# Optimization experiments

Hardware: AMD Instinct MI355X
Metric: run time of the kernel (lower is better)

## Reference

```python
import jax, jax.numpy as jnp
import numpy as np

B, C, H, W = 8, 64, 256, 256
SQ = 256  # max(int(64*16*0.25),1)

def setup_inputs() -> dict:
    key = jax.random.key(0)
    k1, k2, k3, k4, k5 = jax.random.split(key, 5)
    t = jax.random.normal(k1, (B, C, H, W), dtype=jnp.float32)
    reduce_w = jax.random.normal(k2, (SQ, 16 * C), dtype=jnp.float32) * (1.0 / np.sqrt(16 * C))
    reduce_b = jax.random.normal(k3, (SQ,), dtype=jnp.float32) * 0.01
    expand_w = jax.random.normal(k4, (16 * C, SQ), dtype=jnp.float32) * (1.0 / np.sqrt(SQ))
    expand_b = jax.random.normal(k5, (16 * C,), dtype=jnp.float32) * 0.01
    return {"t": t, "reduce_w": reduce_w, "reduce_b": reduce_b,
            "expand_w": expand_w, "expand_b": expand_b}

def _mish(x):
    return x * jnp.tanh(jax.nn.softplus(x))

def reference(t, reduce_w, reduce_b, expand_w, expand_b):
    b, c, h, w = t.shape  # h, w assumed multiples of 4 (no pad needed)
    gh, gw = h // 4, w // 4
    # split into 4x4 grid of patches: [B, C, 4, gh, 4, gw]
    tg = t.reshape(b, c, 4, gh, 4, gw)
    # global avg pool per patch -> [B, C, 4, 4]; reorder to cat order (i*4+j)*C + c
    pooled = tg.mean(axis=(3, 5))                      # [B, C, 4, 4]
    pooled = pooled.transpose(0, 2, 3, 1).reshape(b, 16 * c)  # [B, 16C]
    # squeeze-excite MLP (1x1 convs on [B,16C,1,1] == linear layers)
    s = _mish(pooled @ reduce_w.T + reduce_b)          # [B, SQ]
    g = jax.nn.sigmoid(s @ expand_w.T + expand_b)      # [B, 16C]
    # gates back to grid: [B, 4, 4, C] -> [B, C, 4, 1, 4, 1]
    gates = g.reshape(b, 4, 4, c).transpose(0, 3, 1, 2)[:, :, :, None, :, None]
    out = (tg * gates).reshape(b, c, h, w)
    return out
```

## Files before the change

kernel.cpp:

```cpp
#include <hip/hip_runtime.h>
#include <math.h>


#define Bsz 8
#define Csz 64
#define Hsz 256
#define Wsz 256
#define SQsz 256
#define C16 1024

__global__ __launch_bounds__(256) void pool_kernel(const float* __restrict__ t,
                                                   float* __restrict__ pooled) {
    int bid = blockIdx.x;
    int p   = bid & 15;
    int bc  = bid >> 4;
    int i   = p >> 2, j = p & 3;
    const float* base = t + (((size_t)bc * Hsz + (size_t)i * 64) * Wsz + (size_t)j * 64);
    int tid = threadIdx.x;
    float sum = 0.f;
#pragma unroll
    for (int k = 0; k < 4; ++k) {
        int g    = tid + k * 256;
        int row  = g >> 4;
        int col4 = g & 15;
        float4 v = *(const float4*)(base + (size_t)row * Wsz + col4 * 4);
        sum += v.x + v.y + v.z + v.w;
    }
#pragma unroll
    for (int off = 32; off > 0; off >>= 1) sum += __shfl_down(sum, off, 64);
    __shared__ float wsum[4];
    if ((tid & 63) == 0) wsum[tid >> 6] = sum;
    __syncthreads();
    if (tid == 0) {
        float s = wsum[0] + wsum[1] + wsum[2] + wsum[3];
        int b = bc >> 6;
        int c = bc & 63;
        pooled[b * C16 + p * Csz + c] = s * (1.0f / 4096.0f);
    }
}

__global__ __launch_bounds__(64) void reduce_kernel(const float* __restrict__ pooled,
                                                    const float* __restrict__ reduce_w,
                                                    const float* __restrict__ reduce_b,
                                                    float* __restrict__ s_out) {
    int o = blockIdx.x;
    int l = threadIdx.x;
    const float* wrow = reduce_w + (size_t)o * C16;
    float acc[Bsz] = {0.f, 0.f, 0.f, 0.f, 0.f, 0.f, 0.f, 0.f};
#pragma unroll
    for (int m = 0; m < 16; ++m) {
        int k = l + 64 * m;
        float wv = wrow[k];
#pragma unroll
        for (int b = 0; b < Bsz; ++b)
            acc[b] = fmaf(wv, pooled[b * C16 + k], acc[b]);
    }
#pragma unroll
    for (int off = 32; off > 0; off >>= 1) {
#pragma unroll
        for (int b = 0; b < Bsz; ++b)
            acc[b] += __shfl_xor(acc[b], off, 64);
    }
    if (l < Bsz) {
        float x = acc[l] + reduce_b[o];
        float sp = (x > 15.f) ? x : log1pf(expf(x));
        s_out[l * SQsz + o] = x * tanhf(sp);
    }
}

__global__ __launch_bounds__(64) void expand_kernel(const float* __restrict__ s_in,
                                                    const float* __restrict__ expand_w,
                                                    const float* __restrict__ expand_b,
                                                    float* __restrict__ g_out) {
    int o = blockIdx.x;
    int l = threadIdx.x;
    const float* wrow = expand_w + (size_t)o * SQsz;
    float acc[Bsz] = {0.f, 0.f, 0.f, 0.f, 0.f, 0.f, 0.f, 0.f};
#pragma unroll
    for (int m = 0; m < 4; ++m) {
        int k = l + 64 * m;
        float wv = wrow[k];
#pragma unroll
        for (int b = 0; b < Bsz; ++b)
            acc[b] = fmaf(wv, s_in[b * SQsz + k], acc[b]);
    }
#pragma unroll
    for (int off = 32; off > 0; off >>= 1) {
#pragma unroll
        for (int b = 0; b < Bsz; ++b)
            acc[b] += __shfl_xor(acc[b], off, 64);
    }
    if (l < Bsz) {
        float x = acc[l] + expand_b[o];
        g_out[l * C16 + o] = 1.0f / (1.0f + expf(-x));
    }
}

__global__ __launch_bounds__(256) void scale_kernel(const float* __restrict__ t,
                                                    const float* __restrict__ g,
                                                    float* __restrict__ out) {
    unsigned int idx = blockIdx.x * 256u + threadIdx.x;
    int w4 = idx & 63;
    int h  = (idx >> 6) & 255;
    int c  = (idx >> 14) & 63;
    int b  = idx >> 20;
    int p  = ((h >> 6) << 2) | (w4 >> 4);
    float gate = g[(b << 10) + (p << 6) + c];
    float4 v = *(const float4*)(t + (size_t)idx * 4);
    float4 r;
    r.x = v.x * gate;
    r.y = v.y * gate;
    r.z = v.z * gate;
    r.w = v.w * gate;
    *(float4*)(out + (size_t)idx * 4) = r;
}

extern "C" void kernel_launch(void* const* d_in, const int* in_sizes, int n_in,
                              void* d_out, int out_size, void* d_ws, size_t ws_size,
                              hipStream_t stream) {
    const float* t        = (const float*)d_in[0];
    const float* reduce_w = (const float*)d_in[1];
    const float* reduce_b = (const float*)d_in[2];
    const float* expand_w = (const float*)d_in[3];
    const float* expand_b = (const float*)d_in[4];
    float* out = (float*)d_out;

    float* pooled = (float*)d_ws;
    float* s_buf  = pooled + Bsz * C16;
    float* g_buf  = s_buf + Bsz * SQsz;

    pool_kernel  <<<Bsz * Csz * 16, 256, 0, stream>>>(t, pooled);
    reduce_kernel<<<SQsz,            64, 0, stream>>>(pooled, reduce_w, reduce_b, s_buf);
    expand_kernel<<<C16,             64, 0, stream>>>(s_buf, expand_w, expand_b, g_buf);
    scale_kernel <<<32768,          256, 0, stream>>>(t, g_buf, out);
}
```

Measured before the change: 257.5 us.

## Widen MLP kernels to one thread per input and use nontemporal scale loads/stores

The reduce and expand matvec kernels now give each thread a single input element (1024 and 256 threads per block) and combine the per-wave partial sums through shared memory, instead of running a serial 16- or 4-step loop in one wave. This shortens per-block latency on these small serial stages. The scale kernel switches to nontemporal vector loads and stores for the streamed tensor, so it is meant to pollute the cache less. The trade-off is that the input tensor may already be cached from the pooling pass, and nontemporal loads could bypass that reuse.

After: 260.4 us. Within noise of the previous version (+1.1%).

```diff
diff --git a/kernel.cpp b/kernel.cpp
--- a/kernel.cpp
+++ b/kernel.cpp
@@ -8,6 +8,8 @@
 #define Wsz 256
 #define SQsz 256
 #define C16 1024
+
+typedef float f32x4 __attribute__((ext_vector_type(4)));
 
 __global__ __launch_bounds__(256) void pool_kernel(const float* __restrict__ t,
                                                    float* __restrict__ pooled) {
@@ -23,7 +25,7 @@
         int g    = tid + k * 256;
         int row  = g >> 4;
         int col4 = g & 15;
-        float4 v = *(const float4*)(base + (size_t)row * Wsz + col4 * 4);
+        f32x4 v = *(const f32x4*)(base + (size_t)row * Wsz + col4 * 4);
         sum += v.x + v.y + v.z + v.w;
     }
 #pragma unroll
@@ -39,60 +41,68 @@
     }
 }
 
-__global__ __launch_bounds__(64) void reduce_kernel(const float* __restrict__ pooled,
-                                                    const float* __restrict__ reduce_w,
-                                                    const float* __restrict__ reduce_b,
-                                                    float* __restrict__ s_out) {
-    int o = blockIdx.x;
-    int l = threadIdx.x;
-    const float* wrow = reduce_w + (size_t)o * C16;
-    float acc[Bsz] = {0.f, 0.f, 0.f, 0.f, 0.f, 0.f, 0.f, 0.f};
+__global__ __launch_bounds__(1024) void reduce_kernel(const float* __restrict__ pooled,
+                                                      const float* __restrict__ reduce_w,
+                                                      const float* __restrict__ reduce_b,
+                                                      float* __restrict__ s_out) {
+    int o   = blockIdx.x;
+    int tid = threadIdx.x;
+    int w   = tid >> 6;
+    int l   = tid & 63;
+    float wv = reduce_w[(size_t)o * C16 + tid];
+    float acc[Bsz];
 #pragma unroll
-    for (int m = 0; m < 16; ++m) {
-        int k = l + 64 * m;
-        float wv = wrow[k];
-#pragma unroll
-        for (int b = 0; b < Bsz; ++b)
-            acc[b] = fmaf(wv, pooled[b * C16 + k], acc[b]);
-    }
+    for (int b = 0; b < Bsz; ++b)
+        acc[b] = wv * pooled[b * C16 + tid];
 #pragma unroll
     for (int off = 32; off > 0; off >>= 1) {
 #pragma unroll
         for (int b = 0; b < Bsz; ++b)
             acc[b] += __shfl_xor(acc[b], off, 64);
     }
-    if (l < Bsz) {
-        float x = acc[l] + reduce_b[o];
+    __shared__ float red[16][Bsz];
+    if (l == 0) {
+#pragma unroll
+        for (int b = 0; b < Bsz; ++b) red[w][b] = acc[b];
+    }
+    __syncthreads();
+    if (tid < Bsz) {
+        float x = reduce_b[o];
+#pragma unroll
+        for (int q = 0; q < 16; ++q) x += red[q][tid];
         float sp = (x > 15.f) ? x : log1pf(expf(x));
-        s_out[l * SQsz + o] = x * tanhf(sp);
+        s_out[tid * SQsz + o] = x * tanhf(sp);
     }
 }
 
-__global__ __launch_bounds__(64) void expand_kernel(const float* __restrict__ s_in,
-                                                    const float* __restrict__ expand_w,
-                                                    const float* __restrict__ expand_b,
-                                                    float* __restrict__ g_out) {
-    int o = blockIdx.x;
-    int l = threadIdx.x;
-    const float* wrow = expand_w + (size_t)o * SQsz;
-    float acc[Bsz] = {0.f, 0.f, 0.f, 0.f, 0.f, 0.f, 0.f, 0.f};
+__global__ __launch_bounds__(256) void expand_kernel(const float* __restrict__ s_in,
+                                                     const float* __restrict__ expand_w,
+                                                     const float* __restrict__ expand_b,
+                                                     float* __restrict__ g_out) {
+    int o   = blockIdx.x;
+    int tid = threadIdx.x;
+    int w   = tid >> 6;
+    int l   = tid & 63;
+    float wv = expand_w[(size_t)o * SQsz + tid];
+    float acc[Bsz];
 #pragma unroll
-    for (int m = 0; m < 4; ++m) {
-        int k = l + 64 * m;
-        float wv = wrow[k];
-#pragma unroll
-        for (int b = 0; b < Bsz; ++b)
-            acc[b] = fmaf(wv, s_in[b * SQsz + k], acc[b]);
-    }
+    for (int b = 0; b < Bsz; ++b)
+        acc[b] = wv * s_in[b * SQsz + tid];
 #pragma unroll
     for (int off = 32; off > 0; off >>= 1) {
 #pragma unroll
         for (int b = 0; b < Bsz; ++b)
             acc[b] += __shfl_xor(acc[b], off, 64);
     }
-    if (l < Bsz) {
-        float x = acc[l] + expand_b[o];
-        g_out[l * C16 + o] = 1.0f / (1.0f + expf(-x));
+    __shared__ float red[4][Bsz];
+    if (l == 0) {
+#pragma unroll
+        for (int b = 0; b < Bsz; ++b) red[w][b] = acc[b];
+    }
+    __syncthreads();
+    if (tid < Bsz) {
+        float x = expand_b[o] + red[0][tid] + red[1][tid] + red[2][tid] + red[3][tid];
+        g_out[tid * C16 + o] = 1.0f / (1.0f + expf(-x));
     }
 }
 
@@ -106,13 +116,13 @@
     int b  = idx >> 20;
     int p  = ((h >> 6) << 2) | (w4 >> 4);
     float gate = g[(b << 10) + (p << 6) + c];
-    float4 v = *(const float4*)(t + (size_t)idx * 4);
-    float4 r;
+    f32x4 v = __builtin_nontemporal_load((const f32x4*)(t + (size_t)idx * 4));
+    f32x4 r;
     r.x = v.x * gate;
     r.y = v.y * gate;
     r.z = v.z * gate;
     r.w = v.w * gate;
-    *(float4*)(out + (size_t)idx * 4) = r;
+    __builtin_nontemporal_store(r, (f32x4*)(out + (size_t)idx * 4));
 }
 
 extern "C" void kernel_launch(void* const* d_in, const int* in_sizes, int n_in,
@@ -130,7 +140,7 @@
     float* g_buf  = s_buf + Bsz * SQsz;
 
     pool_kernel  <<<Bsz * Csz * 16, 256, 0, stream>>>(t, pooled);
-    reduce_kernel<<<SQsz,            64, 0, stream>>>(pooled, reduce_w, reduce_b, s_buf);
-    expand_kernel<<<C16,             64, 0, stream>>>(s_buf, expand_w, expand_b, g_buf);
+    reduce_kernel<<<SQsz,          1024, 0, stream>>>(pooled, reduce_w, reduce_b, s_buf);
+    expand_kernel<<<C16,            256, 0, stream>>>(s_buf, expand_w, expand_b, g_buf);
     scale_kernel <<<32768,          256, 0, stream>>>(t, g_buf, out);
 }
```
